# Performance work log

Hardware: AMD Instinct MI355X
Metric: run time of the kernel (lower is better)

Reference implementation:

```python
import jax, jax.numpy as jnp
import numpy as np

N = 4096          # n_nodes
M = 8192          # m_nodes (= 2*N, required by block structure)
D = 128           # in_dim == hidden_dim (conv1 is reapplied to its own output)
H = 128
NUM_ITERS = 3


def setup_inputs() -> dict:
    key = jax.random.key(0)
    ks = jax.random.split(key, 6)
    X = jax.random.normal(ks[0], (N, D), dtype=jnp.float32)
    R = jax.random.uniform(ks[1], (N, N), dtype=jnp.float32)
    A = 0.5 * (R + R.T)  # symmetric, strictly positive connectivity matrix
    # upsample MLP: Linear(n_nodes -> m_nodes - n_nodes), torch weight layout [out, in]
    W_up = jax.random.normal(ks[2], (M - N, N), dtype=jnp.float32) * 0.02
    b_up = jnp.zeros((M - N,), dtype=jnp.float32)
    # GCNConv linear weights stored [in, out]
    W1 = jax.random.normal(ks[3], (D, H), dtype=jnp.float32) * 0.05
    b1 = jnp.zeros((H,), dtype=jnp.float32)
    W2 = jax.random.normal(ks[4], (H, H), dtype=jnp.float32) * 0.05
    b2 = jnp.zeros((H,), dtype=jnp.float32)
    return dict(X=X, A=A, W_up=W_up, b_up=b_up, W1=W1, b1=b1, W2=W2, b2=b2)


def _gcn(Adj, X, W, b):
    # PyG GCNConv on a fully dense, strictly-positive weighted graph:
    # every diagonal entry is nonzero, so add_remaining_self_loops is a no-op and
    # out = D^{-1/2} A D^{-1/2} (X W) + b  exactly.
    deg = Adj.sum(axis=0)                         # [m] column degree
    dinv = jnp.where(deg > 0, jax.lax.rsqrt(deg), 0.0)
    An = Adj * dinv[:, None] * dinv[None, :]      # symmetric normalization
    return An @ (X @ W) + b


def reference(X, A, W_up, b_up, W1, b1, W2, b2):
    # new_nodes = upsample_mlp(X.T).T  -> [M-N, D]
    new_nodes = (X.T @ W_up.T + b_up).T
    Xu = jnp.concatenate([X, new_nodes], axis=0)  # [M, D]
    # block adjacency: [[A, A.T], [A, sigmoid(new @ new.T)]]
    Adj = jnp.block([[A, A.T],
                     [A, jax.nn.sigmoid(new_nodes @ new_nodes.T)]])  # [M, M]
    A_out = Adj
    for _ in range(NUM_ITERS):
        Xu = jax.nn.relu(_gcn(Adj, Xu, W1, b1))
        Adj = jax.nn.sigmoid(Xu @ Xu.T)           # mid-loop adjacency rebuild
        Xu = jax.nn.relu(_gcn(Adj, Xu, W2, b2))
        A_out = jax.nn.sigmoid(Xu @ Xu.T)
        # NOTE: edge_index for the next conv1 is NOT rebuilt from A_out in the
        # original (only after conv1), so Adj carries the mid-loop matrix.
    return A_out
```

## Files before the change

### kernel.cpp

```cpp
#include <hip/hip_runtime.h>
#include <hip/hip_bf16.h>


#define N_NODES 4096
#define M_NODES 8192
#define DIM 128
#define SLICE_ELEMS ((size_t)M_NODES * DIM)

typedef __attribute__((ext_vector_type(4))) float f32x4;
typedef __attribute__((ext_vector_type(8))) short bf16x8;

__device__ __forceinline__ unsigned short f2bf(float f) {
  union { float f; unsigned u; } v; v.f = f;
  unsigned r = v.u + 0x7fffu + ((v.u >> 16) & 1u);
  return (unsigned short)(r >> 16);
}

__device__ __forceinline__ void gld16(unsigned short* lds, const unsigned short* g) {
  __builtin_amdgcn_global_load_lds(
      (const __attribute__((address_space(1))) unsigned int*)g,
      (__attribute__((address_space(3))) unsigned int*)lds, 16, 0, 0);
}

__device__ __forceinline__ float sigmoidf_(float x) { return 1.0f / (1.0f + __expf(-x)); }


__global__ void cast_x_kernel(const float* __restrict__ X, unsigned short* __restrict__ Xu,
                              unsigned short* __restrict__ XT) {
  int idx = blockIdx.x * 256 + threadIdx.x;
  int i = idx >> 7, c = idx & 127;
  unsigned short b = f2bf(X[idx]);
  Xu[idx] = b;
  XT[(size_t)c * N_NODES + i] = b;
}

__global__ void cast_wup_kernel(const float4* __restrict__ W, unsigned short* __restrict__ Wb) {
  int idx4 = blockIdx.x * 256 + threadIdx.x;
  int r = idx4 >> 10, c = (idx4 & 1023) << 2;
  float4 v = W[idx4];
  ushort4 o;
  o.x = f2bf(v.x); o.y = f2bf(v.y); o.z = f2bf(v.z); o.w = f2bf(v.w);
  int tm = r >> 7, rr = r & 127;
  int kc = c >> 10, st = (c & 1023) >> 5, e = c & 31;
  *(ushort4*)&Wb[((size_t)tm * 4 + kc) * 131072 + (size_t)st * 4096 + rr * 32 + e] = o;
}

__global__ void cast_wt_kernel(const float* __restrict__ W, unsigned short* __restrict__ WT) {
  int idx = blockIdx.x * 256 + threadIdx.x;
  int k = idx >> 7, c = idx & 127;
  WT[c * DIM + k] = f2bf(W[idx]);
}

__global__ void cast_a_kernel(const float* __restrict__ A, unsigned short* __restrict__ Adj,
                              float* __restrict__ colsumA) {
  int c = blockIdx.x * 256 + threadIdx.x;
  int r0 = blockIdx.y * 128;
  int tm = r0 >> 7;
  int kc = c >> 10, st = (c & 1023) >> 5, e = c & 31;
  size_t a1 = ((size_t)(tm)      * 8 + kc)     * 131072 + (size_t)st * 4096 + e;
  size_t a2 = ((size_t)(tm)      * 8 + 4 + kc) * 131072 + (size_t)st * 4096 + e;
  size_t a3 = ((size_t)(tm + 32) * 8 + kc)     * 131072 + (size_t)st * 4096 + e;
  float s = 0.f;
  for (int r = 0; r < 128; ++r) {
    float a = A[(size_t)(r0 + r) * N_NODES + c];
    unsigned short b = f2bf(a);
    Adj[a1 + r * 32] = b; Adj[a2 + r * 32] = b; Adj[a3 + r * 32] = b;
    s += a;
  }
  atomicAdd(&colsumA[c], s);
}

__global__ void init_deg_kernel(const float* __restrict__ colsumA, float* __restrict__ deg) {
  int i = blockIdx.x * 256 + threadIdx.x;
  deg[i] = (i < N_NODES) ? 2.0f * colsumA[i] : colsumA[i - N_NODES];
}

__global__ void dinv_kernel(const float* __restrict__ deg, float* __restrict__ dinv) {
  int i = blockIdx.x * 256 + threadIdx.x;
  float d = deg[i];
  dinv[i] = d > 0.f ? rsqrtf(d) : 0.f;
}


__global__ __launch_bounds__(256, 2)
void agg_kernel(const unsigned short* __restrict__ At, long tileRowElems,
                const unsigned short* __restrict__ BT, long ldb,
                float* __restrict__ accBase, int kIters) {
  __shared__ __align__(16) unsigned short lA[4096];
  __shared__ __align__(16) unsigned short lB[4096];
  const int t = threadIdx.x, w = t >> 6, lane = t & 63;
  const int q = lane >> 4, l15 = lane & 15;
  const int sg0 = blockIdx.y * kIters;
  const size_t abase = (size_t)blockIdx.x * tileRowElems +
                       (size_t)(sg0 >> 5) * 131072 + (size_t)(sg0 & 31) * 4096;
  const size_t bk = (size_t)sg0 * 32;
  const int arow = t >> 2, achk = t & 3;

  f32x4 acc[2][8];
#pragma unroll
  for (int a = 0; a < 2; ++a)
#pragma unroll
    for (int b = 0; b < 8; ++b) acc[a][b] = (f32x4)0.f;

  for (int s = 0; s < kIters; ++s) {
    __syncthreads();
    gld16(&lA[t * 8],        &At[abase + (size_t)s * 4096 + t * 8]);
    gld16(&lA[2048 + t * 8], &At[abase + (size_t)s * 4096 + 2048 + t * 8]);
    gld16(&lB[t * 8],        &BT[(size_t)arow * ldb + bk + s * 32 + achk * 8]);
    gld16(&lB[2048 + t * 8], &BT[(size_t)(64 + arow) * ldb + bk + s * 32 + achk * 8]);
    __syncthreads();
    bf16x8 a0 = *(const bf16x8*)&lA[(w * 32 + l15) * 32 + q * 8];
    bf16x8 a1 = *(const bf16x8*)&lA[(w * 32 + 16 + l15) * 32 + q * 8];
#pragma unroll
    for (int nt = 0; nt < 8; ++nt) {
      bf16x8 b = *(const bf16x8*)&lB[(nt * 16 + l15) * 32 + q * 8];
      acc[0][nt] = __builtin_amdgcn_mfma_f32_16x16x32_bf16(a0, b, acc[0][nt], 0, 0, 0);
      acc[1][nt] = __builtin_amdgcn_mfma_f32_16x16x32_bf16(a1, b, acc[1][nt], 0, 0, 0);
    }
  }
  float* ct = accBase + (size_t)blockIdx.y * SLICE_ELEMS + (size_t)blockIdx.x * 16384;
#pragma unroll
  for (int mt = 0; mt < 2; ++mt)
#pragma unroll
    for (int nt = 0; nt < 8; ++nt)
      *(f32x4*)&ct[(((w * 2 + mt) * 8 + nt) * 256) + (q * 16 + l15) * 4] = acc[mt][nt];
}

__global__ void reduce_acc_kernel(const float* __restrict__ acc,
                                  unsigned short* __restrict__ dst,
                                  const float* __restrict__ bias_row,
                                  const float* __restrict__ bias_col,
                                  const float* __restrict__ dinv, int mode, int nSlices) {
  int p = blockIdx.x * 256 + threadIdx.x;
  float s = 0.f;
  for (int sp = 0; sp < nSlices; ++sp) s += acc[(size_t)sp * SLICE_ELEMS + p];
  int tile = p >> 14, r = p & 16383;
  int grp = r >> 8, r2 = r & 255;
  int nt = grp & 7, wmt = grp >> 3;
  int i = r2 & 3, ql = r2 >> 2;
  int row = tile * 128 + (wmt >> 1) * 32 + (wmt & 1) * 16 + (ql >> 4) * 4 + i;
  int col = nt * 16 + (ql & 15);
  float v = (mode == 0) ? (s + bias_row[row])
                        : fmaxf(dinv[row] * s + bias_col[col], 0.f);
  dst[(size_t)row * DIM + col] = f2bf(v);
}


template <int MODE>
__global__ __launch_bounds__(256)
void rebuild_kernel(const unsigned short* __restrict__ XA,
                    const unsigned short* __restrict__ XB,
                    void* __restrict__ out, long p1 ,
                    long col0, float* __restrict__ deg) {
  __shared__ __align__(16) unsigned short smem[32768];
  __shared__ float lcol[128];
  unsigned short* lA = smem;
  unsigned short* lB = smem + 16384;
  const int t = threadIdx.x, w = t >> 6, lane = t & 63;
  const int q = lane >> 4, l15 = lane & 15;
  const int i0 = blockIdx.x * 128, j0 = blockIdx.y * 128;
  const int srow = t >> 2, schk = t & 3;
#pragma unroll
  for (int kk = 0; kk < 4; ++kk)
#pragma unroll
    for (int h = 0; h < 2; ++h) {
      gld16(&lA[kk * 4096 + h * 2048 + t * 8],
            &XA[(size_t)(i0 + h * 64 + srow) * DIM + kk * 32 + schk * 8]);
      gld16(&lB[kk * 4096 + h * 2048 + t * 8],
            &XB[(size_t)(j0 + h * 64 + srow) * DIM + kk * 32 + schk * 8]);
    }
  if (MODE == 0 && t < 128) lcol[t] = 0.f;
  __syncthreads();

  f32x4 acc[2][8];
#pragma unroll
  for (int a = 0; a < 2; ++a)
#pragma unroll
    for (int b = 0; b < 8; ++b) acc[a][b] = (f32x4)0.f;

#pragma unroll
  for (int kk = 0; kk < 4; ++kk) {
    bf16x8 a0 = *(const bf16x8*)&lA[kk * 4096 + (w * 32 + l15) * 32 + q * 8];
    bf16x8 a1 = *(const bf16x8*)&lA[kk * 4096 + (w * 32 + 16 + l15) * 32 + q * 8];
#pragma unroll
    for (int nt = 0; nt < 8; ++nt) {
      bf16x8 b = *(const bf16x8*)&lB[kk * 4096 + (nt * 16 + l15) * 32 + q * 8];
      acc[0][nt] = __builtin_amdgcn_mfma_f32_16x16x32_bf16(a0, b, acc[0][nt], 0, 0, 0);
      acc[1][nt] = __builtin_amdgcn_mfma_f32_16x16x32_bf16(a1, b, acc[1][nt], 0, 0, 0);
    }
  }
  __syncthreads();

  if (MODE == 0) {
    unsigned short* lC = smem;
#pragma unroll
    for (int mt = 0; mt < 2; ++mt)
#pragma unroll
      for (int nt = 0; nt < 8; ++nt) {
        float cs = 0.f;
#pragma unroll
        for (int i = 0; i < 4; ++i) {
          float sv = sigmoidf_(acc[mt][nt][i]);
          cs += sv;
          lC[(w * 32 + mt * 16 + q * 4 + i) * 136 + nt * 16 + l15] = f2bf(sv);
        }
        cs += __shfl_xor(cs, 16);
        cs += __shfl_xor(cs, 32);
        if (lane < 16) atomicAdd(&lcol[nt * 16 + lane], cs);
      }
    __syncthreads();
    unsigned short* og = (unsigned short*)out;
    const long rowbase = p1 + i0, colbase = col0 + j0;
    const size_t tb = ((size_t)(rowbase >> 7) * 8 + (colbase >> 10)) * 131072;
    const int stb = (int)((colbase & 1023) >> 5);
#pragma unroll
    for (int cc = 0; cc < 8; ++cc) {
      int ch = t + cc * 256;
      int row = ch >> 4, c16 = ch & 15;
      *(bf16x8*)&og[tb + (size_t)(stb + (c16 >> 2)) * 4096 + row * 32 + (c16 & 3) * 8] =
          *(const bf16x8*)&lC[row * 136 + c16 * 8];
    }
    if (t < 128) atomicAdd(&deg[colbase + t], lcol[t]);
  } else {
    float* og = (float*)out;
    float* lCf = (float*)smem;
#pragma unroll
    for (int h2 = 0; h2 < 2; ++h2) {
      __syncthreads();
      if ((w >> 1) == h2) {
#pragma unroll
        for (int mt = 0; mt < 2; ++mt)
#pragma unroll
          for (int nt = 0; nt < 8; ++nt)
#pragma unroll
            for (int i = 0; i < 4; ++i)
              lCf[((w & 1) * 32 + mt * 16 + q * 4 + i) * 128 + nt * 16 + l15] =
                  sigmoidf_(acc[mt][nt][i]);
      }
      __syncthreads();
#pragma unroll
      for (int j = 0; j < 8; ++j) {
        int ch = t + j * 256;
        int r64 = ch >> 5, c4 = (ch & 31) * 4;
        *(f32x4*)&og[(size_t)(i0 + h2 * 64 + r64) * p1 + j0 + c4] =
            *(const f32x4*)&lCf[r64 * 128 + c4];
      }
    }
  }
}


__global__ __launch_bounds__(256)
void yz_kernel(const unsigned short* __restrict__ Xu, const unsigned short* __restrict__ WT,
               const float* __restrict__ dinv, unsigned short* __restrict__ ZT, int ldz) {
  __shared__ __align__(16) unsigned short smem[32768];
  unsigned short* lA = smem;
  unsigned short* lB = smem + 16384;
  const int t = threadIdx.x, w = t >> 6, lane = t & 63;
  const int q = lane >> 4, l15 = lane & 15;
  const int r0 = blockIdx.x * 128;
  const int srow = t >> 2, schk = t & 3;
#pragma unroll
  for (int kk = 0; kk < 4; ++kk)
#pragma unroll
    for (int h = 0; h < 2; ++h) {
      gld16(&lA[kk * 4096 + h * 2048 + t * 8],
            &Xu[(size_t)(r0 + h * 64 + srow) * DIM + kk * 32 + schk * 8]);
      gld16(&lB[kk * 4096 + h * 2048 + t * 8],
            &WT[(size_t)(h * 64 + srow) * DIM + kk * 32 + schk * 8]);
    }
  __syncthreads();

  f32x4 acc[2][8];
#pragma unroll
  for (int a = 0; a < 2; ++a)
#pragma unroll
    for (int b = 0; b < 8; ++b) acc[a][b] = (f32x4)0.f;

#pragma unroll
  for (int kk = 0; kk < 4; ++kk) {
    bf16x8 a0 = *(const bf16x8*)&lA[kk * 4096 + (w * 32 + l15) * 32 + q * 8];
    bf16x8 a1 = *(const bf16x8*)&lA[kk * 4096 + (w * 32 + 16 + l15) * 32 + q * 8];
#pragma unroll
    for (int nt = 0; nt < 8; ++nt) {
      bf16x8 b = *(const bf16x8*)&lB[kk * 4096 + (nt * 16 + l15) * 32 + q * 8];
      acc[0][nt] = __builtin_amdgcn_mfma_f32_16x16x32_bf16(a0, b, acc[0][nt], 0, 0, 0);
      acc[1][nt] = __builtin_amdgcn_mfma_f32_16x16x32_bf16(a1, b, acc[1][nt], 0, 0, 0);
    }
  }
  __syncthreads();
  unsigned short* lT = smem;
#pragma unroll
  for (int mt = 0; mt < 2; ++mt)
#pragma unroll
    for (int nt = 0; nt < 8; ++nt)
#pragma unroll
      for (int i = 0; i < 4; ++i) {
        int r = w * 32 + mt * 16 + q * 4 + i;
        lT[(nt * 16 + l15) * 136 + r] = f2bf(dinv[r0 + r] * acc[mt][nt][i]);
      }
  __syncthreads();
#pragma unroll
  for (int cc = 0; cc < 8; ++cc) {
    int ch = t + cc * 256;
    int c = ch >> 4, c16 = ch & 15;
    *(bf16x8*)&ZT[(size_t)c * ldz + r0 + c16 * 8] = *(const bf16x8*)&lT[c * 136 + c16 * 8];
  }
}


extern "C" void kernel_launch(void* const* d_in, const int* in_sizes, int n_in,
                              void* d_out, int out_size, void* d_ws, size_t ws_size,
                              hipStream_t stream) {
  (void)in_sizes; (void)n_in; (void)out_size;
  const float* X   = (const float*)d_in[0];
  const float* A   = (const float*)d_in[1];
  const float* Wup = (const float*)d_in[2];
  const float* bup = (const float*)d_in[3];
  const float* W1  = (const float*)d_in[4];
  const float* b1  = (const float*)d_in[5];
  const float* W2  = (const float*)d_in[6];
  const float* b2  = (const float*)d_in[7];

  const size_t ADJ_BYTES = (size_t)M_NODES * M_NODES * 2;
  char* ws = (char*)d_ws;
  size_t off = 0;
  auto alloc = [&](size_t bytes) {
    char* p = ws + off;
    off += (bytes + 255) & ~(size_t)255;
    return p;
  };
  float*          accb    = (float*)alloc(8 * SLICE_ELEMS * 4);
  unsigned short* Xu      = (unsigned short*)alloc((size_t)M_NODES * DIM * 2);
  unsigned short* ZT      = (unsigned short*)alloc((size_t)DIM * M_NODES * 2);
  unsigned short* XT      = (unsigned short*)alloc((size_t)DIM * N_NODES * 2);
  unsigned short* W1T     = (unsigned short*)alloc(DIM * DIM * 2);
  unsigned short* W2T     = (unsigned short*)alloc(DIM * DIM * 2);
  float*          colsumA = (float*)alloc(N_NODES * 4);
  float*          deg     = (float*)alloc(M_NODES * 4);
  float*          dinv    = (float*)alloc(M_NODES * 4);

  unsigned short* Adj;
  if (ws_size >= off + ADJ_BYTES) Adj = (unsigned short*)(ws + off);
  else                            Adj = (unsigned short*)d_out;
  unsigned short* Wupb = Adj;

  unsigned short* XuNew = Xu + (size_t)N_NODES * DIM;

  hipMemsetAsync(colsumA, 0, N_NODES * 4, stream);
  cast_x_kernel<<<N_NODES * DIM / 256, 256, 0, stream>>>(X, Xu, XT);
  cast_wup_kernel<<<((size_t)N_NODES * N_NODES / 4) / 256, 256, 0, stream>>>(
      (const float4*)Wup, Wupb);
  cast_wt_kernel<<<64, 256, 0, stream>>>(W1, W1T);
  cast_wt_kernel<<<64, 256, 0, stream>>>(W2, W2T);

  agg_kernel<<<dim3(N_NODES / 128, 8), 256, 0, stream>>>(
      Wupb, 4L * 131072, XT, N_NODES, accb, 16);
  reduce_acc_kernel<<<N_NODES * DIM / 256, 256, 0, stream>>>(
      accb, XuNew, bup, nullptr, nullptr, 0, 8);

  cast_a_kernel<<<dim3(N_NODES / 256, N_NODES / 128), 256, 0, stream>>>(A, Adj, colsumA);
  init_deg_kernel<<<M_NODES / 256, 256, 0, stream>>>(colsumA, deg);
  rebuild_kernel<0><<<dim3(N_NODES / 128, N_NODES / 128), 256, 0, stream>>>(
      XuNew, XuNew, Adj, N_NODES, N_NODES, deg);
  dinv_kernel<<<M_NODES / 256, 256, 0, stream>>>(deg, dinv);

  for (int it = 0; it < 3; ++it) {
    yz_kernel<<<M_NODES / 128, 256, 0, stream>>>(Xu, W1T, dinv, ZT, M_NODES);
    agg_kernel<<<dim3(M_NODES / 128, 8), 256, 0, stream>>>(
        Adj, 8L * 131072, ZT, M_NODES, accb, 32);
    reduce_acc_kernel<<<M_NODES * DIM / 256, 256, 0, stream>>>(
        accb, Xu, nullptr, b1, dinv, 1, 8);
    hipMemsetAsync(deg, 0, M_NODES * 4, stream);
    rebuild_kernel<0><<<dim3(M_NODES / 128, M_NODES / 128), 256, 0, stream>>>(
        Xu, Xu, Adj, 0, 0, deg);
    dinv_kernel<<<M_NODES / 256, 256, 0, stream>>>(deg, dinv);
    yz_kernel<<<M_NODES / 128, 256, 0, stream>>>(Xu, W2T, dinv, ZT, M_NODES);
    agg_kernel<<<dim3(M_NODES / 128, 8), 256, 0, stream>>>(
        Adj, 8L * 131072, ZT, M_NODES, accb, 32);
    reduce_acc_kernel<<<M_NODES * DIM / 256, 256, 0, stream>>>(
        accb, Xu, nullptr, b2, dinv, 1, 8);
    if (it == 2)
      rebuild_kernel<1><<<dim3(M_NODES / 128, M_NODES / 128), 256, 0, stream>>>(
          Xu, Xu, d_out, M_NODES, 0, nullptr);
  }
}
```

Measured before the change: 989.1 us.

## Triple-buffer agg_kernel loads, fold dinv into consumers, merge weight casts

Triple-buffers the A/B tiles in agg_kernel so global-to-LDS loads run two steps ahead, using explicit vmcnt waits and raw barriers instead of two syncthreads per step. It removes the dinv kernel by computing rsqrt(deg) inline in yz and reduce, merges the two weight-cast launches into one, and doubles the split-K slices for the upsample GEMM to expose more parallelism. The costs are more LDS per block, which may lower occupancy, a larger accumulator workspace, and extra reduction work. The abase formula is simplified in a way that assumes contiguous k-slabs.

```diff
diff --git a/kernel.cpp b/kernel.cpp
--- a/kernel.cpp
+++ b/kernel.cpp
@@ -45,10 +45,15 @@
   *(ushort4*)&Wb[((size_t)tm * 4 + kc) * 131072 + (size_t)st * 4096 + rr * 32 + e] = o;
 }
 
-__global__ void cast_wt_kernel(const float* __restrict__ W, unsigned short* __restrict__ WT) {
+__global__ void cast_wt2_kernel(const float* __restrict__ W1, const float* __restrict__ W2,
+                                unsigned short* __restrict__ WT1,
+                                unsigned short* __restrict__ WT2) {
   int idx = blockIdx.x * 256 + threadIdx.x;
-  int k = idx >> 7, c = idx & 127;
-  WT[c * DIM + k] = f2bf(W[idx]);
+  const float* W = idx < 16384 ? W1 : W2;
+  unsigned short* WT = idx < 16384 ? WT1 : WT2;
+  int j = idx & 16383;
+  int k = j >> 7, c = j & 127;
+  WT[c * DIM + k] = f2bf(W[j]);
 }
 
 __global__ void cast_a_kernel(const float* __restrict__ A, unsigned short* __restrict__ Adj,
@@ -75,48 +80,62 @@
   deg[i] = (i < N_NODES) ? 2.0f * colsumA[i] : colsumA[i - N_NODES];
 }
 
-__global__ void dinv_kernel(const float* __restrict__ deg, float* __restrict__ dinv) {
-  int i = blockIdx.x * 256 + threadIdx.x;
-  float d = deg[i];
-  dinv[i] = d > 0.f ? rsqrtf(d) : 0.f;
-}
-
 
 __global__ __launch_bounds__(256, 2)
 void agg_kernel(const unsigned short* __restrict__ At, long tileRowElems,
                 const unsigned short* __restrict__ BT, long ldb,
                 float* __restrict__ accBase, int kIters) {
-  __shared__ __align__(16) unsigned short lA[4096];
-  __shared__ __align__(16) unsigned short lB[4096];
+  __shared__ __align__(16) unsigned short smem[24576];
   const int t = threadIdx.x, w = t >> 6, lane = t & 63;
   const int q = lane >> 4, l15 = lane & 15;
   const int sg0 = blockIdx.y * kIters;
-  const size_t abase = (size_t)blockIdx.x * tileRowElems +
-                       (size_t)(sg0 >> 5) * 131072 + (size_t)(sg0 & 31) * 4096;
+  const size_t abase = (size_t)blockIdx.x * tileRowElems + (size_t)sg0 * 4096;
   const size_t bk = (size_t)sg0 * 32;
   const int arow = t >> 2, achk = t & 3;
 
+  auto STAGE = [&](int s, int b) {
+    unsigned short* la = smem + b * 8192;
+    unsigned short* lb = la + 4096;
+    gld16(&la[t * 8],        &At[abase + (size_t)s * 4096 + t * 8]);
+    gld16(&la[2048 + t * 8], &At[abase + (size_t)s * 4096 + 2048 + t * 8]);
+    gld16(&lb[t * 8],        &BT[(size_t)arow * ldb + bk + s * 32 + achk * 8]);
+    gld16(&lb[2048 + t * 8], &BT[(size_t)(64 + arow) * ldb + bk + s * 32 + achk * 8]);
+  };
+
   f32x4 acc[2][8];
 #pragma unroll
   for (int a = 0; a < 2; ++a)
 #pragma unroll
     for (int b = 0; b < 8; ++b) acc[a][b] = (f32x4)0.f;
 
+  STAGE(0, 0);
+  if (kIters > 1) STAGE(1, 1);
+
   for (int s = 0; s < kIters; ++s) {
-    __syncthreads();
-    gld16(&lA[t * 8],        &At[abase + (size_t)s * 4096 + t * 8]);
-    gld16(&lA[2048 + t * 8], &At[abase + (size_t)s * 4096 + 2048 + t * 8]);
-    gld16(&lB[t * 8],        &BT[(size_t)arow * ldb + bk + s * 32 + achk * 8]);
-    gld16(&lB[2048 + t * 8], &BT[(size_t)(64 + arow) * ldb + bk + s * 32 + achk * 8]);
-    __syncthreads();
-    bf16x8 a0 = *(const bf16x8*)&lA[(w * 32 + l15) * 32 + q * 8];
-    bf16x8 a1 = *(const bf16x8*)&lA[(w * 32 + 16 + l15) * 32 + q * 8];
+    if (s + 2 < kIters) {
+      STAGE(s + 2, (s + 2) % 3);
+      asm volatile("s_waitcnt vmcnt(8)" ::: "memory");
+    } else if (s + 1 < kIters) {
+      asm volatile("s_waitcnt vmcnt(4)" ::: "memory");
+    } else {
+      asm volatile("s_waitcnt vmcnt(0)" ::: "memory");
+    }
+    __builtin_amdgcn_s_barrier();
+    __builtin_amdgcn_sched_barrier(0);
+
+    const unsigned short* la = smem + (s % 3) * 8192;
+    const unsigned short* lb = la + 4096;
+    bf16x8 a0 = *(const bf16x8*)&la[(w * 32 + l15) * 32 + q * 8];
+    bf16x8 a1 = *(const bf16x8*)&la[(w * 32 + 16 + l15) * 32 + q * 8];
 #pragma unroll
     for (int nt = 0; nt < 8; ++nt) {
-      bf16x8 b = *(const bf16x8*)&lB[(nt * 16 + l15) * 32 + q * 8];
+      bf16x8 b = *(const bf16x8*)&lb[(nt * 16 + l15) * 32 + q * 8];
       acc[0][nt] = __builtin_amdgcn_mfma_f32_16x16x32_bf16(a0, b, acc[0][nt], 0, 0, 0);
       acc[1][nt] = __builtin_amdgcn_mfma_f32_16x16x32_bf16(a1, b, acc[1][nt], 0, 0, 0);
     }
+    __builtin_amdgcn_sched_barrier(0);
+    __builtin_amdgcn_s_barrier();
+    __builtin_amdgcn_sched_barrier(0);
   }
   float* ct = accBase + (size_t)blockIdx.y * SLICE_ELEMS + (size_t)blockIdx.x * 16384;
 #pragma unroll
@@ -130,7 +149,7 @@
                                   unsigned short* __restrict__ dst,
                                   const float* __restrict__ bias_row,
                                   const float* __restrict__ bias_col,
-                                  const float* __restrict__ dinv, int mode, int nSlices) {
+                                  const float* __restrict__ deg, int mode, int nSlices) {
   int p = blockIdx.x * 256 + threadIdx.x;
   float s = 0.f;
   for (int sp = 0; sp < nSlices; ++sp) s += acc[(size_t)sp * SLICE_ELEMS + p];
@@ -140,8 +159,14 @@
   int i = r2 & 3, ql = r2 >> 2;
   int row = tile * 128 + (wmt >> 1) * 32 + (wmt & 1) * 16 + (ql >> 4) * 4 + i;
   int col = nt * 16 + (ql & 15);
-  float v = (mode == 0) ? (s + bias_row[row])
-                        : fmaxf(dinv[row] * s + bias_col[col], 0.f);
+  float v;
+  if (mode == 0) {
+    v = s + bias_row[row];
+  } else {
+    float d = deg[row];
+    float dv = d > 0.f ? rsqrtf(d) : 0.f;
+    v = fmaxf(dv * s + bias_col[col], 0.f);
+  }
   dst[(size_t)row * DIM + col] = f2bf(v);
 }
 
@@ -252,7 +277,7 @@
 
 __global__ __launch_bounds__(256)
 void yz_kernel(const unsigned short* __restrict__ Xu, const unsigned short* __restrict__ WT,
-               const float* __restrict__ dinv, unsigned short* __restrict__ ZT, int ldz) {
+               const float* __restrict__ deg, unsigned short* __restrict__ ZT, int ldz) {
   __shared__ __align__(16) unsigned short smem[32768];
   unsigned short* lA = smem;
   unsigned short* lB = smem + 16384;
@@ -293,12 +318,14 @@
 #pragma unroll
   for (int mt = 0; mt < 2; ++mt)
 #pragma unroll
-    for (int nt = 0; nt < 8; ++nt)
-#pragma unroll
-      for (int i = 0; i < 4; ++i) {
-        int r = w * 32 + mt * 16 + q * 4 + i;
-        lT[(nt * 16 + l15) * 136 + r] = f2bf(dinv[r0 + r] * acc[mt][nt][i]);
-      }
+    for (int i = 0; i < 4; ++i) {
+      int r = w * 32 + mt * 16 + q * 4 + i;
+      float d = deg[r0 + r];
+      float dv = d > 0.f ? rsqrtf(d) : 0.f;
+#pragma unroll
+      for (int nt = 0; nt < 8; ++nt)
+        lT[(nt * 16 + l15) * 136 + r] = f2bf(dv * acc[mt][nt][i]);
+    }
   __syncthreads();
 #pragma unroll
   for (int cc = 0; cc < 8; ++cc) {
@@ -330,7 +357,7 @@
     off += (bytes + 255) & ~(size_t)255;
     return p;
   };
-  float*          accb    = (float*)alloc(8 * SLICE_ELEMS * 4);
+  float*          accb    = (float*)alloc(16 * SLICE_ELEMS * 4);
   unsigned short* Xu      = (unsigned short*)alloc((size_t)M_NODES * DIM * 2);
   unsigned short* ZT      = (unsigned short*)alloc((size_t)DIM * M_NODES * 2);
   unsigned short* XT      = (unsigned short*)alloc((size_t)DIM * N_NODES * 2);
@@ -338,7 +365,6 @@
   unsigned short* W2T     = (unsigned short*)alloc(DIM * DIM * 2);
   float*          colsumA = (float*)alloc(N_NODES * 4);
   float*          deg     = (float*)alloc(M_NODES * 4);
-  float*          dinv    = (float*)alloc(M_NODES * 4);
 
   unsigned short* Adj;
   if (ws_size >= off + ADJ_BYTES) Adj = (unsigned short*)(ws + off);
@@ -351,35 +377,32 @@
   cast_x_kernel<<<N_NODES * DIM / 256, 256, 0, stream>>>(X, Xu, XT);
   cast_wup_kernel<<<((size_t)N_NODES * N_NODES / 4) / 256, 256, 0, stream>>>(
       (const float4*)Wup, Wupb);
-  cast_wt_kernel<<<64, 256, 0, stream>>>(W1, W1T);
-  cast_wt_kernel<<<64, 256, 0, stream>>>(W2, W2T);
-
-  agg_kernel<<<dim3(N_NODES / 128, 8), 256, 0, stream>>>(
-      Wupb, 4L * 131072, XT, N_NODES, accb, 16);
+  cast_wt2_kernel<<<128, 256, 0, stream>>>(W1, W2, W1T, W2T);
+
+  agg_kernel<<<dim3(N_NODES / 128, 16), 256, 0, stream>>>(
+      Wupb, 4L * 131072, XT, N_NODES, accb, 8);
   reduce_acc_kernel<<<N_NODES * DIM / 256, 256, 0, stream>>>(
-      accb, XuNew, bup, nullptr, nullptr, 0, 8);
+      accb, XuNew, bup, nullptr, nullptr, 0, 16);
 
   cast_a_kernel<<<dim3(N_NODES / 256, N_NODES / 128), 256, 0, stream>>>(A, Adj, colsumA);
   init_deg_kernel<<<M_NODES / 256, 256, 0, stream>>>(colsumA, deg);
   rebuild_kernel<0><<<dim3(N_NODES / 128, N_NODES / 128), 256, 0, stream>>>(
       XuNew, XuNew, Adj, N_NODES, N_NODES, deg);
-  dinv_kernel<<<M_NODES / 256, 256, 0, stream>>>(deg, dinv);
 
   for (int it = 0; it < 3; ++it) {
-    yz_kernel<<<M_NODES / 128, 256, 0, stream>>>(Xu, W1T, dinv, ZT, M_NODES);
+    yz_kernel<<<M_NODES / 128, 256, 0, stream>>>(Xu, W1T, deg, ZT, M_NODES);
     agg_kernel<<<dim3(M_NODES / 128, 8), 256, 0, stream>>>(
         Adj, 8L * 131072, ZT, M_NODES, accb, 32);
     reduce_acc_kernel<<<M_NODES * DIM / 256, 256, 0, stream>>>(
-        accb, Xu, nullptr, b1, dinv, 1, 8);
+        accb, Xu, nullptr, b1, deg, 1, 8);
     hipMemsetAsync(deg, 0, M_NODES * 4, stream);
     rebuild_kernel<0><<<dim3(M_NODES / 128, M_NODES / 128), 256, 0, stream>>>(
         Xu, Xu, Adj, 0, 0, deg);
-    dinv_kernel<<<M_NODES / 256, 256, 0, stream>>>(deg, dinv);
-    yz_kernel<<<M_NODES / 128, 256, 0, stream>>>(Xu, W2T, dinv, ZT, M_NODES);
+    yz_kernel<<<M_NODES / 128, 256, 0, stream>>>(Xu, W2T, deg, ZT, M_NODES);
     agg_kernel<<<dim3(M_NODES / 128, 8), 256, 0, stream>>>(
         Adj, 8L * 131072, ZT, M_NODES, accb, 32);
     reduce_acc_kernel<<<M_NODES * DIM / 256, 256, 0, stream>>>(
-        accb, Xu, nullptr, b2, dinv, 1, 8);
+        accb, Xu, nullptr, b2, deg, 1, 8);
     if (it == 2)
       rebuild_kernel<1><<<dim3(M_NODES / 128, M_NODES / 128), 256, 0, stream>>>(
           Xu, Xu, d_out, M_NODES, 0, nullptr);
```

After: 974.7 us. Within noise of the previous version (-1.5%).
